# Kernel tuning notes

Measured on AMD Instinct MI355X. Metric: run time of the kernel, lower is better.

The kernel has to match this reference:

```python
import jax, jax.numpy as jnp
import numpy as np

B, T, E, N, V = 256, 256, 64, 512, 128  # batch, T_x, emb_dim, n_a, n_unique


def setup_inputs() -> dict:
    key = jax.random.key(0)
    ks = jax.random.split(key, 6)
    scale = 0.05
    X = jax.random.randint(ks[0], (B, T), 0, V, dtype=jnp.int32)
    h_0 = jnp.zeros((B, N), jnp.float32)
    c_0 = jnp.zeros((B, N), jnp.float32)
    emb = jax.random.normal(ks[1], (V, E), jnp.float32) * scale   # char-emb-layer
    Wx = jax.random.normal(ks[2], (E, 4 * N), jnp.float32) * scale  # LSTM kernel (i,f,c,o)
    Wh = jax.random.normal(ks[3], (N, 4 * N), jnp.float32) * scale  # LSTM recurrent kernel
    b = jnp.concatenate([jnp.zeros((N,)), jnp.ones((N,)), jnp.zeros((2 * N,))]).astype(jnp.float32)  # unit forget bias
    Wd = jax.random.normal(ks[4], (N, V), jnp.float32) * scale     # final dense kernel
    bd = jnp.zeros((V,), jnp.float32)
    return {"X": X, "h_0": h_0, "c_0": c_0, "emb": emb, "Wx": Wx, "Wh": Wh, "b": b, "Wd": Wd, "bd": bd}


def _lstm_scan(xz, h_0, c_0, Wh):
    # xz: [T, B, 4N] precomputed input projections (+bias)
    def step(carry, z_x):
        h, c = carry
        z = z_x + h @ Wh
        i, f, g, o = jnp.split(z, 4, axis=-1)  # Keras gate order: i, f, c(g), o
        i = jax.nn.sigmoid(i)
        f = jax.nn.sigmoid(f)
        g = jnp.tanh(g)
        o = jax.nn.sigmoid(o)
        c = f * c + i * g
        h = o * jnp.tanh(c)
        return (h, c), h

    (_, _), hs = jax.lax.scan(step, (h_0, c_0), xz)
    return hs  # [T, B, N]


def reference(X, h_0, c_0, emb, Wx, Wh, b, Wd, bd):
    xs = emb[X]                                   # [B, T, E] embedding lookup
    xz = jnp.einsum('bte,eg->tbg', xs, Wx) + b    # fold input GEMM out of the recurrence
    hs = _lstm_scan(xz, h_0, c_0, Wh)             # [T, B, N]
    logits = jnp.einsum('tbn,nv->btv', hs, Wd) + bd  # [B, T, V]
    return logits
```

## Files before the change

kernel.cpp:

```cpp
#include <hip/hip_runtime.h>

#define Bb 256
#define Tt 256
#define Ee 64
#define Nn 512
#define Vv 128
#define Gg 2048

typedef __attribute__((ext_vector_type(8))) _Float16 fp16x8;
typedef __attribute__((ext_vector_type(4))) float f32x4;

__device__ __forceinline__ unsigned short f2h(float f) {
  union { _Float16 h; unsigned short u; } cv;
  cv.h = (_Float16)f;
  return cv.u;
}

__device__ __forceinline__ unsigned long long ldg_agent(const unsigned long long* p) {
  return __hip_atomic_load(p, __ATOMIC_RELAXED, __HIP_MEMORY_SCOPE_AGENT);
}
__device__ __forceinline__ void stg_agent(unsigned int* p, unsigned int v) {
  __hip_atomic_store(p, v, __ATOMIC_RELAXED, __HIP_MEMORY_SCOPE_AGENT);
}

__device__ __forceinline__ float sigm_fast(float x) { return 1.f / (1.f + __expf(-x)); }
__device__ __forceinline__ float tanh_fast(float x) { return 1.f - 2.f / (1.f + __expf(2.f * x)); }

__global__ void proj_kernel(const float* __restrict__ emb, const float* __restrict__ Wx,
                            const float* __restrict__ bias, float* __restrict__ proj,
                            unsigned int* __restrict__ ctr) {
  const int v = blockIdx.x;
  __shared__ float el[Ee];
  if (threadIdx.x < Ee) el[threadIdx.x] = emb[v * Ee + threadIdx.x];
  __syncthreads();
  for (int g = threadIdx.x; g < Gg; g += blockDim.x) {
    float s = bias[g];
#pragma unroll
    for (int e = 0; e < Ee; ++e) s = fmaf(el[e], Wx[e * Gg + g], s);
    proj[v * Gg + g] = s;
  }
  if (v == 0) ctr[threadIdx.x] = 0u;
}

__launch_bounds__(512, 2)
__global__ void lstm_kernel(const int* __restrict__ X, const float* __restrict__ h0,
                            const float* __restrict__ c0, const float* __restrict__ Wh,
                            const float* __restrict__ Wd, const float* __restrict__ bd,
                            const float* __restrict__ proj, unsigned short* __restrict__ hx,
                            unsigned int* __restrict__ ctr, float* __restrict__ out) {
  extern __shared__ char smem[];
  short* Whs = (short*)smem;
  short* hl  = (short*)smem;
  float* zl  = (float*)(smem + 32768);
  float* dl  = (float*)(smem + 41472);
  float* Wdl = (float*)(smem + 45568);

  const int tid = threadIdx.x;
  const int bg = blockIdx.x & 7;
  const int nc = blockIdx.x >> 3;
  const int nbase = nc << 4;
  const int vbase = nc << 2;
  const int grow0 = bg << 5;

  for (int i = tid; i < 64 * 512; i += 512) {
    int col = i & 63;
    int k = i >> 6;
    int zc = (col >> 4) * Nn + nbase + (col & 15);
    unsigned short w = f2h(Wh[k * Gg + zc]);
    int unit = col * 64 + ((k >> 3) ^ (col & 7));
    ((unsigned short*)Whs)[unit * 8 + (k & 7)] = w;
  }
  __syncthreads();

  const int w = tid >> 6, lane = tid & 63;
  const int btile = w & 1, gate = w >> 1;
  const int arow = (btile << 4) + (lane & 15);
  const int bcol = (gate << 4) + (lane & 15);
  const int kg = lane >> 4;

  fp16x8 bfrag[16];
#pragma unroll
  for (int ks = 0; ks < 16; ++ks) {
    int slot = ks * 4 + kg;
    bfrag[ks] = ((const fp16x8*)Whs)[bcol * 64 + (slot ^ (bcol & 7))];
  }
  __syncthreads();

  for (int i = tid; i < 2048; i += 512) {
    int k = i >> 2, dvv = i & 3;
    Wdl[k * 5 + dvv] = Wd[k * Vv + vbase + dvv];
  }

  const int ub = tid >> 4;
  const int un = tid & 15;
  float c = c0[(grow0 + ub) * Nn + nbase + un];

  const int db = tid >> 4, dv = (tid >> 2) & 3, dq = tid & 3;
  const float bdv = bd[vbase + (tid & 3)];
  const int* xrow = X + (grow0 + ub) * Tt;
  unsigned int* const myctr = &ctr[bg * 32];

#pragma unroll 1
  for (int t = 0; t < Tt; ++t) {
    const int curb = t & 1;

    const int vch = xrow[t];
    const float* pr = proj + (size_t)vch * Gg + nbase + un;
    const float p_i = pr[0 * Nn], p_f = pr[1 * Nn], p_g = pr[2 * Nn], p_o = pr[3 * Nn];

    if (t == 0) {
#pragma unroll
      for (int ci = tid; ci < 2048; ci += 512) {
        int row = ci >> 6, slot = ci & 63;
        const float* src = h0 + (grow0 + row) * Nn + slot * 8;
        fp16x8 v;
#pragma unroll
        for (int j = 0; j < 8; ++j) v[j] = (_Float16)src[j];
        ((fp16x8*)hl)[row * 64 + (slot ^ (row & 7))] = v;
      }
    } else {
      const unsigned long long* src =
          (const unsigned long long*)hx + (((size_t)(curb ^ 1) * Bb * Nn) >> 2);
#pragma unroll
      for (int ci = tid; ci < 2048; ci += 512) {
        int row = ci >> 6, slot = ci & 63;
        const unsigned long long* p = src + ((size_t)(grow0 + row) * 64 + slot) * 2;
        unsigned long long lo = ldg_agent(p);
        unsigned long long hi = ldg_agent(p + 1);
        unsigned long long* d =
            (unsigned long long*)hl + ((size_t)row * 64 + (slot ^ (row & 7))) * 2;
        d[0] = lo;
        d[1] = hi;
      }
    }
    __syncthreads();

    f32x4 a0 = {0.f, 0.f, 0.f, 0.f}, a1 = {0.f, 0.f, 0.f, 0.f};
    f32x4 a2 = {0.f, 0.f, 0.f, 0.f}, a3 = {0.f, 0.f, 0.f, 0.f};
#pragma unroll
    for (int ks = 0; ks < 16; ks += 4) {
      fp16x8 h0v = ((const fp16x8*)hl)[arow * 64 + (((ks + 0) * 4 + kg) ^ (arow & 7))];
      fp16x8 h1v = ((const fp16x8*)hl)[arow * 64 + (((ks + 1) * 4 + kg) ^ (arow & 7))];
      fp16x8 h2v = ((const fp16x8*)hl)[arow * 64 + (((ks + 2) * 4 + kg) ^ (arow & 7))];
      fp16x8 h3v = ((const fp16x8*)hl)[arow * 64 + (((ks + 3) * 4 + kg) ^ (arow & 7))];
      a0 = __builtin_amdgcn_mfma_f32_16x16x32_f16(h0v, bfrag[ks + 0], a0, 0, 0, 0);
      a1 = __builtin_amdgcn_mfma_f32_16x16x32_f16(h1v, bfrag[ks + 1], a1, 0, 0, 0);
      a2 = __builtin_amdgcn_mfma_f32_16x16x32_f16(h2v, bfrag[ks + 2], a2, 0, 0, 0);
      a3 = __builtin_amdgcn_mfma_f32_16x16x32_f16(h3v, bfrag[ks + 3], a3, 0, 0, 0);
    }
#pragma unroll
    for (int j = 0; j < 4; ++j)
      zl[((btile << 4) + ((lane >> 4) << 2) + j) * 68 + (gate << 4) + (lane & 15)] =
          (a0[j] + a1[j]) + (a2[j] + a3[j]);
    __syncthreads();

    {
      float zi = zl[ub * 68 + 0 + un] + p_i;
      float zf = zl[ub * 68 + 16 + un] + p_f;
      float zg = zl[ub * 68 + 32 + un] + p_g;
      float zo = zl[ub * 68 + 48 + un] + p_o;
      float ii = sigm_fast(zi);
      float ff = sigm_fast(zf);
      float gg = tanh_fast(zg);
      float oo = sigm_fast(zo);
      c = ff * c + ii * gg;
      float h = oo * tanh_fast(c);
      unsigned int hb = f2h(h);
      unsigned int nb = __shfl_xor(hb, 1);
      if (!(lane & 1)) {
        size_t off = (size_t)curb * Bb * Nn + (size_t)(grow0 + ub) * Nn + nbase + un;
        stg_agent((unsigned int*)hx + (off >> 1), hb | (nb << 16));
      }
    }
    __syncthreads();

    if (tid == 0) {
      __hip_atomic_fetch_add(myctr, 1u, __ATOMIC_RELAXED, __HIP_MEMORY_SCOPE_AGENT);
    }
    if (t >= 2 && tid < 128) {
      const float* dlR = dl + (t & 1) * 512;
      float s = dlR[tid * 4] + dlR[tid * 4 + 1] + dlR[tid * 4 + 2] + dlR[tid * 4 + 3] + bdv;
      __builtin_nontemporal_store(
          s, &out[((size_t)(grow0 + (tid >> 2)) * Tt + (t - 2)) * Vv + vbase + (tid & 3)]);
    }
    if (t >= 1) {
      const unsigned long long* hlq = (const unsigned long long*)hl;
      float s0 = 0.f, s1 = 0.f, s2 = 0.f, s3 = 0.f;
#pragma unroll 8
      for (int m = 0; m < 32; ++m) {
        int u = dq + (m << 2);
        int sx = (u >> 1) ^ (db & 7);
        union { unsigned long long q; _Float16 h4[4]; } r;
        r.q = hlq[(((size_t)db << 6) + sx) * 2 + (u & 1)];
        int wb = 20 * u + dv;
        s0 = fmaf((float)r.h4[0], Wdl[wb + 0], s0);
        s1 = fmaf((float)r.h4[1], Wdl[wb + 5], s1);
        s2 = fmaf((float)r.h4[2], Wdl[wb + 10], s2);
        s3 = fmaf((float)r.h4[3], Wdl[wb + 15], s3);
      }
      dl[((t + 1) & 1) * 512 + tid] = (s0 + s1) + (s2 + s3);
    }
    if (tid == 0) {
      const unsigned int tgt = 32u * (unsigned int)(t + 1);
      while (__hip_atomic_load(myctr, __ATOMIC_RELAXED, __HIP_MEMORY_SCOPE_AGENT) < tgt) {
        __builtin_amdgcn_s_sleep(1);
      }
    }
    __syncthreads();
  }

  {
    if (tid < 128) {
      float s = dl[tid * 4] + dl[tid * 4 + 1] + dl[tid * 4 + 2] + dl[tid * 4 + 3] + bdv;
      __builtin_nontemporal_store(
          s, &out[((size_t)(grow0 + (tid >> 2)) * Tt + (Tt - 2)) * Vv + vbase + (tid & 3)]);
    }
    const unsigned long long* hq = (const unsigned long long*)hx +
                                   (((size_t)((Tt - 1) & 1) * Bb * Nn) >> 2) +
                                   ((size_t)(grow0 + db) * Nn >> 2);
    float s0 = 0.f, s1 = 0.f, s2 = 0.f, s3 = 0.f;
#pragma unroll 8
    for (int m = 0; m < 32; ++m) {
      int u = dq + (m << 2);
      union { unsigned long long q; _Float16 h4[4]; } r;
      r.q = ldg_agent(&hq[u]);
      int wb = 20 * u + dv;
      s0 = fmaf((float)r.h4[0], Wdl[wb + 0], s0);
      s1 = fmaf((float)r.h4[1], Wdl[wb + 5], s1);
      s2 = fmaf((float)r.h4[2], Wdl[wb + 10], s2);
      s3 = fmaf((float)r.h4[3], Wdl[wb + 15], s3);
    }
    dl[512 + tid] = (s0 + s1) + (s2 + s3);
    __syncthreads();
    if (tid < 128) {
      float s = dl[512 + tid * 4] + dl[512 + tid * 4 + 1] + dl[512 + tid * 4 + 2] +
                dl[512 + tid * 4 + 3] + bdv;
      __builtin_nontemporal_store(
          s, &out[((size_t)(grow0 + (tid >> 2)) * Tt + (Tt - 1)) * Vv + vbase + (tid & 3)]);
    }
  }
}

extern "C" void kernel_launch(void* const* d_in, const int* in_sizes, int n_in,
                              void* d_out, int out_size, void* d_ws, size_t ws_size,
                              hipStream_t stream) {
  const int* X = (const int*)d_in[0];
  const float* h0 = (const float*)d_in[1];
  const float* c0 = (const float*)d_in[2];
  const float* emb = (const float*)d_in[3];
  const float* Wx = (const float*)d_in[4];
  const float* Wh = (const float*)d_in[5];
  const float* bias = (const float*)d_in[6];
  const float* Wd = (const float*)d_in[7];
  const float* bd = (const float*)d_in[8];
  float* out = (float*)d_out;

  float* proj = (float*)d_ws;
  unsigned short* hx = (unsigned short*)(proj + Vv * Gg);
  unsigned int* ctr = (unsigned int*)(hx + 2 * Bb * Nn);

  proj_kernel<<<dim3(Vv), dim3(256), 0, stream>>>(emb, Wx, bias, proj, ctr);

  void* args[] = {(void*)&X,  (void*)&h0,   (void*)&c0, (void*)&Wh, (void*)&Wd,
                  (void*)&bd, (void*)&proj, (void*)&hx, (void*)&ctr, (void*)&out};
  hipLaunchCooperativeKernel((const void*)lstm_kernel, dim3(256), dim3(512), args,
                             (unsigned int)65536, stream);
}
```

Before: 1.378 ms.

## Use per-block flag array barrier, 64-bit h stores, and fp16 dot2 for output projection

The per-step grid barrier changes from a single atomic counter incremented by each block to a per-block flag array. Each block writes its step number, and one wavefront polls all 32 flags in parallel and waits until every flag reaches the target. Hidden-state writes are packed into 64-bit stores after two shuffles. The dense output projection stores Wd as packed fp16 pairs and uses the fdot2 instruction, which lowers accumulation precision slightly in exchange for fewer FMAs and less LDS traffic. The change aims to remove atomic contention and serialization on the inter-block sync that is paid every timestep.

```diff
diff --git a/kernel.cpp b/kernel.cpp
--- a/kernel.cpp
+++ b/kernel.cpp
@@ -8,7 +8,17 @@
 #define Gg 2048
 
 typedef __attribute__((ext_vector_type(8))) _Float16 fp16x8;
+typedef __attribute__((ext_vector_type(2))) _Float16 h2;
 typedef __attribute__((ext_vector_type(4))) float f32x4;
+
+#if defined(__has_builtin)
+#if __has_builtin(__builtin_amdgcn_fdot2)
+#define FDOT2(a, b, c) __builtin_amdgcn_fdot2((a), (b), (c), false)
+#endif
+#endif
+#ifndef FDOT2
+#define FDOT2(a, b, c) fmaf((float)(a)[0], (float)(b)[0], fmaf((float)(a)[1], (float)(b)[1], (c)))
+#endif
 
 __device__ __forceinline__ unsigned short f2h(float f) {
   union { _Float16 h; unsigned short u; } cv;
@@ -19,7 +29,13 @@
 __device__ __forceinline__ unsigned long long ldg_agent(const unsigned long long* p) {
   return __hip_atomic_load(p, __ATOMIC_RELAXED, __HIP_MEMORY_SCOPE_AGENT);
 }
-__device__ __forceinline__ void stg_agent(unsigned int* p, unsigned int v) {
+__device__ __forceinline__ unsigned int ldg_agent32(const unsigned int* p) {
+  return __hip_atomic_load(p, __ATOMIC_RELAXED, __HIP_MEMORY_SCOPE_AGENT);
+}
+__device__ __forceinline__ void stg_agent32(unsigned int* p, unsigned int v) {
+  __hip_atomic_store(p, v, __ATOMIC_RELAXED, __HIP_MEMORY_SCOPE_AGENT);
+}
+__device__ __forceinline__ void stg_agent64(unsigned long long* p, unsigned long long v) {
   __hip_atomic_store(p, v, __ATOMIC_RELAXED, __HIP_MEMORY_SCOPE_AGENT);
 }
 
@@ -53,7 +69,7 @@
   short* hl  = (short*)smem;
   float* zl  = (float*)(smem + 32768);
   float* dl  = (float*)(smem + 41472);
-  float* Wdl = (float*)(smem + 45568);
+  unsigned int* Wdh = (unsigned int*)(smem + 45568);
 
   const int tid = threadIdx.x;
   const int bg = blockIdx.x & 7;
@@ -86,9 +102,12 @@
   }
   __syncthreads();
 
-  for (int i = tid; i < 2048; i += 512) {
-    int k = i >> 2, dvv = i & 3;
-    Wdl[k * 5 + dvv] = Wd[k * Vv + vbase + dvv];
+  for (int i = tid; i < 1024; i += 512) {
+    int u = i >> 3, p = (i >> 2) & 1, dvv = i & 3;
+    int k0 = 4 * u + 2 * p;
+    unsigned int lo = f2h(Wd[k0 * Vv + vbase + dvv]);
+    unsigned int hi = f2h(Wd[(k0 + 1) * Vv + vbase + dvv]);
+    Wdh[u * 10 + p * 5 + dvv] = lo | (hi << 16);
   }
 
   const int ub = tid >> 4;
@@ -98,7 +117,7 @@
   const int db = tid >> 4, dv = (tid >> 2) & 3, dq = tid & 3;
   const float bdv = bd[vbase + (tid & 3)];
   const int* xrow = X + (grow0 + ub) * Tt;
-  unsigned int* const myctr = &ctr[bg * 32];
+  unsigned int* const flags = &ctr[bg * 32];
 
 #pragma unroll 1
   for (int t = 0; t < Tt; ++t) {
@@ -166,17 +185,17 @@
       c = ff * c + ii * gg;
       float h = oo * tanh_fast(c);
       unsigned int hb = f2h(h);
-      unsigned int nb = __shfl_xor(hb, 1);
-      if (!(lane & 1)) {
+      unsigned int v01 = hb | (__shfl_xor(hb, 1) << 16);
+      unsigned long long v03 =
+          (unsigned long long)v01 | ((unsigned long long)__shfl_xor(v01, 2) << 32);
+      if (!(lane & 3)) {
         size_t off = (size_t)curb * Bb * Nn + (size_t)(grow0 + ub) * Nn + nbase + un;
-        stg_agent((unsigned int*)hx + (off >> 1), hb | (nb << 16));
-      }
-    }
-    __syncthreads();
-
-    if (tid == 0) {
-      __hip_atomic_fetch_add(myctr, 1u, __ATOMIC_RELAXED, __HIP_MEMORY_SCOPE_AGENT);
-    }
+        stg_agent64((unsigned long long*)(hx + off), v03);
+      }
+    }
+    __syncthreads();
+
+    if (tid == 0) stg_agent32(&flags[nc], t + 1u);
     if (t >= 2 && tid < 128) {
       const float* dlR = dl + (t & 1) * 512;
       float s = dlR[tid * 4] + dlR[tid * 4 + 1] + dlR[tid * 4 + 2] + dlR[tid * 4 + 3] + bdv;
@@ -185,24 +204,24 @@
     }
     if (t >= 1) {
       const unsigned long long* hlq = (const unsigned long long*)hl;
-      float s0 = 0.f, s1 = 0.f, s2 = 0.f, s3 = 0.f;
+      float s0 = 0.f, s1 = 0.f;
 #pragma unroll 8
       for (int m = 0; m < 32; ++m) {
         int u = dq + (m << 2);
         int sx = (u >> 1) ^ (db & 7);
-        union { unsigned long long q; _Float16 h4[4]; } r;
+        union { unsigned long long q; h2 p[2]; } r;
         r.q = hlq[(((size_t)db << 6) + sx) * 2 + (u & 1)];
-        int wb = 20 * u + dv;
-        s0 = fmaf((float)r.h4[0], Wdl[wb + 0], s0);
-        s1 = fmaf((float)r.h4[1], Wdl[wb + 5], s1);
-        s2 = fmaf((float)r.h4[2], Wdl[wb + 10], s2);
-        s3 = fmaf((float)r.h4[3], Wdl[wb + 15], s3);
-      }
-      dl[((t + 1) & 1) * 512 + tid] = (s0 + s1) + (s2 + s3);
-    }
-    if (tid == 0) {
-      const unsigned int tgt = 32u * (unsigned int)(t + 1);
-      while (__hip_atomic_load(myctr, __ATOMIC_RELAXED, __HIP_MEMORY_SCOPE_AGENT) < tgt) {
+        const h2* wp = (const h2*)(Wdh + u * 10 + dv);
+        s0 = FDOT2(r.p[0], wp[0], s0);
+        s1 = FDOT2(r.p[1], wp[5], s1);
+      }
+      dl[((t + 1) & 1) * 512 + tid] = s0 + s1;
+    }
+    if (w == 0) {
+      const unsigned int tgt = t + 1u;
+      while (true) {
+        unsigned int v = (lane < 32) ? ldg_agent32(&flags[lane]) : tgt;
+        if (__all(v >= tgt)) break;
         __builtin_amdgcn_s_sleep(1);
       }
     }
@@ -218,19 +237,17 @@
     const unsigned long long* hq = (const unsigned long long*)hx +
                                    (((size_t)((Tt - 1) & 1) * Bb * Nn) >> 2) +
                                    ((size_t)(grow0 + db) * Nn >> 2);
-    float s0 = 0.f, s1 = 0.f, s2 = 0.f, s3 = 0.f;
+    float s0 = 0.f, s1 = 0.f;
 #pragma unroll 8
     for (int m = 0; m < 32; ++m) {
       int u = dq + (m << 2);
-      union { unsigned long long q; _Float16 h4[4]; } r;
+      union { unsigned long long q; h2 p[2]; } r;
       r.q = ldg_agent(&hq[u]);
-      int wb = 20 * u + dv;
-      s0 = fmaf((float)r.h4[0], Wdl[wb + 0], s0);
-      s1 = fmaf((float)r.h4[1], Wdl[wb + 5], s1);
-      s2 = fmaf((float)r.h4[2], Wdl[wb + 10], s2);
-      s3 = fmaf((float)r.h4[3], Wdl[wb + 15], s3);
-    }
-    dl[512 + tid] = (s0 + s1) + (s2 + s3);
+      const h2* wp = (const h2*)(Wdh + u * 10 + dv);
+      s0 = FDOT2(r.p[0], wp[0], s0);
+      s1 = FDOT2(r.p[1], wp[5], s1);
+    }
+    dl[512 + tid] = s0 + s1;
     __syncthreads();
     if (tid < 128) {
       float s = dl[512 + tid * 4] + dl[512 + tid * 4 + 1] + dl[512 + tid * 4 + 2] +
```

New measurement: 1.250 ms. -9.3%, faster.
